# Kernel optimization log

Measured on AMD Instinct MI355X. Metric: run time of the kernel, lower is better.

The kernel has to match this reference:

```python
import jax, jax.numpy as jnp
import numpy as np

B, S, T, D = 4, 512, 512, 256


def setup_inputs() -> dict:
    key = jax.random.key(0)
    ks = jax.random.split(key, 10)
    scale = 1.0 / np.sqrt(D)
    return {
        "source": jax.random.normal(ks[0], (B, S, D), jnp.float32),
        "target": jax.random.normal(ks[1], (B, T, D), jnp.float32),
        "W_src": jax.random.uniform(ks[2], (D, D), jnp.float32, -scale, scale),
        "b_src": jax.random.uniform(ks[3], (D,), jnp.float32, -scale, scale),
        "W_tgt": jax.random.uniform(ks[4], (D, D), jnp.float32, -scale, scale),
        "b_tgt": jax.random.uniform(ks[5], (D,), jnp.float32, -scale, scale),
        "W_res": jax.random.uniform(ks[6], (D, 1), jnp.float32, -scale, scale),
        "b_res": jax.random.uniform(ks[7], (1,), jnp.float32, -scale, scale),
        "W_prob": jax.random.uniform(ks[8], (D, 2), jnp.float32, -scale, scale),
        "b_prob": jax.random.uniform(ks[9], (2,), jnp.float32, -scale, scale),
    }


def reference(source, target, W_src, b_src, W_tgt, b_tgt, W_res, b_res, W_prob, b_prob):
    # source: (B,S,D), target: (B,T,D)
    src_lin = jnp.einsum("bsd,de->bse", source, W_src) + b_src  # (B,S,D)
    tgt_lin = jnp.einsum("btd,de->bte", target, W_tgt) + b_tgt  # (B,T,D)
    # Bahdanau-style additive attention: (B,T,S,D) broadcast, tanh, D->1
    h = jnp.tanh(src_lin[:, None, :, :] + tgt_lin[:, :, None, :])  # (B,T,S,D)
    genP = jnp.einsum("btsd,d->bts", h, W_res[:, 0]) + b_res[0]     # (B,T,S)
    prob = jax.nn.softmax(jnp.einsum("btd,de->bte", target, W_prob) + b_prob, axis=-1)  # (B,T,2)
    return genP, prob
```

## Files before the change

kernel.cpp:

```cpp
#include <hip/hip_runtime.h>

#define B_ 4
#define S_ 512
#define T_ 512
#define D_ 256
#define NSRC (B_ * S_)
#define NROW 4096
#define K2F 2.8853900817779268f

typedef __attribute__((ext_vector_type(8))) short short8;
typedef __attribute__((ext_vector_type(4))) float f32x4;
typedef __attribute__((ext_vector_type(2))) float f32x2;

__device__ __forceinline__ unsigned short f2bf(float f) {
    union { float f; unsigned u; } v; v.f = f;
    unsigned r = v.u + 0x7FFF + ((v.u >> 16) & 1);
    return (unsigned short)(r >> 16);
}

__global__ __launch_bounds__(256) void prep_kernel(
    const float* __restrict__ tgt,
    const float* __restrict__ Wsrc, const float* __restrict__ Wtgt,
    const float* __restrict__ Wp, const float* __restrict__ bp,
    unsigned short* __restrict__ wtb, float* __restrict__ out)
{
    __shared__ float tl[64 * 65];
    const int blk = blockIdx.x, tid = threadIdx.x;

    if (blk < 32) {
        int wb = blk;
        int e = wb >> 4, ti = wb & 15, tr = ti >> 2, tc = ti & 3;
        int r0 = tr * 64, c0 = tc * 64;
        const float* W = e ? Wtgt : Wsrc;
        #pragma unroll
        for (int it = 0; it < 4; it++) {
            int rr = (tid >> 4) + it * 16;
            int cc = (tid & 15) * 4;
            float4 v = *(const float4*)&W[(r0 + rr) * D_ + c0 + cc];
            tl[(cc + 0) * 65 + rr] = v.x;
            tl[(cc + 1) * 65 + rr] = v.y;
            tl[(cc + 2) * 65 + rr] = v.z;
            tl[(cc + 3) * 65 + rr] = v.w;
        }
        __syncthreads();
        #pragma unroll
        for (int it = 0; it < 2; it++) {
            int jj = (tid >> 3) + it * 32;
            int kk = (tid & 7) * 8;
            ushort4 lo, hi;
            lo.x = f2bf(tl[jj * 65 + kk + 0]); lo.y = f2bf(tl[jj * 65 + kk + 1]);
            lo.z = f2bf(tl[jj * 65 + kk + 2]); lo.w = f2bf(tl[jj * 65 + kk + 3]);
            hi.x = f2bf(tl[jj * 65 + kk + 4]); hi.y = f2bf(tl[jj * 65 + kk + 5]);
            hi.z = f2bf(tl[jj * 65 + kk + 6]); hi.w = f2bf(tl[jj * 65 + kk + 7]);
            int idx = (e * 256 + c0 + jj) * D_ + r0 + kk;
            *(ushort4*)&wtb[idx] = lo;
            *(ushort4*)&wtb[idx + 4] = hi;
        }
    } else {
        int row  = (blk - 32) * 4 + (tid >> 6);
        int lane = tid & 63;
        float p0 = 0.f, p1 = 0.f;
        #pragma unroll
        for (int i = 0; i < 4; i++) {
            int d = lane + i * 64;
            float v = tgt[row * D_ + d];
            float2 w = *(const float2*)&Wp[d * 2];
            p0 = fmaf(v, w.x, p0);
            p1 = fmaf(v, w.y, p1);
        }
        #pragma unroll
        for (int off = 32; off > 0; off >>= 1) {
            p0 += __shfl_down(p0, off, 64);
            p1 += __shfl_down(p1, off, 64);
        }
        if (lane == 0) {
            const float L2E = 1.4426950408889634f;
            float l0 = p0 + bp[0], l1 = p1 + bp[1];
            float e10 = __builtin_amdgcn_exp2f((l1 - l0) * L2E);
            float e01 = __builtin_amdgcn_exp2f((l0 - l1) * L2E);
            out[B_ * T_ * S_ + row * 2 + 0] = __builtin_amdgcn_rcpf(1.f + e10);
            out[B_ * T_ * S_ + row * 2 + 1] = __builtin_amdgcn_rcpf(1.f + e01);
        }
    }
}

__global__ __launch_bounds__(256) void ysyt_kernel(
    const float* __restrict__ src, const float* __restrict__ tgt,
    const unsigned short* __restrict__ wtb,
    const float* __restrict__ bsrc, const float* __restrict__ btgt,
    float* __restrict__ yst)
{
    const int bx = blockIdx.x;
    const int rowblk = bx >> 2, colq = bx & 3;
    const int R0 = rowblk * 64;
    const int tid = threadIdx.x, lane = tid & 63, w = tid >> 6;
    const int n = lane & 15, quad = lane >> 4;
    const int mat = (R0 >= NSRC) ? 1 : 0;
    const float* bias = mat ? btgt : bsrc;
    const unsigned short* wtbase = wtb + mat * 256 * D_;
    const float* xb = mat ? &tgt[(R0 - NSRC) * D_] : &src[R0 * D_];

    short8 af[8];
    #pragma unroll
    for (int ks = 0; ks < 8; ks++) {
        const float* p = &xb[(w * 16 + n) * D_ + ks * 32 + quad * 8];
        float4 u0 = *(const float4*)p;
        float4 u1 = *(const float4*)(p + 4);
        short8 v;
        v[0] = (short)f2bf(u0.x); v[1] = (short)f2bf(u0.y);
        v[2] = (short)f2bf(u0.z); v[3] = (short)f2bf(u0.w);
        v[4] = (short)f2bf(u1.x); v[5] = (short)f2bf(u1.y);
        v[6] = (short)f2bf(u1.z); v[7] = (short)f2bf(u1.w);
        af[ks] = v;
    }

    #pragma unroll
    for (int gc = 0; gc < 4; gc++) {
        const int gcol = colq * 4 + gc;
        const unsigned short* bptr = &wtbase[(gcol * 16 + n) * D_ + quad * 8];
        short8 bf[8];
        #pragma unroll
        for (int ks = 0; ks < 8; ks++) bf[ks] = *(const short8*)&bptr[ks * 32];
        f32x4 a4 = {0.f, 0.f, 0.f, 0.f};
        #pragma unroll
        for (int ks = 0; ks < 8; ks++)
            a4 = __builtin_amdgcn_mfma_f32_16x16x32_bf16(af[ks], bf[ks], a4, 0, 0, 0);
        const float bv = bias[gcol * 16 + n];
        float4 o;
        o.x = __builtin_amdgcn_exp2f((a4[0] + bv) * K2F);
        o.y = __builtin_amdgcn_exp2f((a4[1] + bv) * K2F);
        o.z = __builtin_amdgcn_exp2f((a4[2] + bv) * K2F);
        o.w = __builtin_amdgcn_exp2f((a4[3] + bv) * K2F);
        *(float4*)&yst[(gcol * 16 + n) * NROW + R0 + w * 16 + quad * 4] = o;
    }
}

#define CLS 36
__global__ __launch_bounds__(256) void genp_kernel(
    const float* __restrict__ yst,
    const float* __restrict__ Wres, const float* __restrict__ bres,
    float* __restrict__ out)
{
    __shared__ float lys[2][64][CLS];
    __shared__ float lyt[2][64][CLS];
    __shared__ float c0s;

    const int tid = threadIdx.x;
    const int lane = tid & 63, w = tid >> 6;
    const int s0 = blockIdx.x * 32;
    const int t0 = blockIdx.y * 32;
    const int b  = blockIdx.z;
    const int m = tid & 15;
    const int g = tid >> 4;
    const int r = tid >> 3;
    const int q = tid & 7;

    if (w == 0) {
        float s = Wres[lane] + Wres[lane + 64] + Wres[lane + 128] + Wres[lane + 192];
        #pragma unroll
        for (int off = 32; off > 0; off >>= 1) s += __shfl_xor(s, off, 64);
        if (lane == 0) c0s = s + bres[0];
    }

    const int ysbase = b * S_ + s0;
    const int ytbase = NSRC + b * T_ + t0;

    {
        float4 a0 = *(const float4*)&yst[(r)      * NROW + ysbase + 4 * q];
        float4 a1 = *(const float4*)&yst[(r + 32) * NROW + ysbase + 4 * q];
        float4 b0 = *(const float4*)&yst[(r)      * NROW + ytbase + 4 * q];
        float4 b1 = *(const float4*)&yst[(r + 32) * NROW + ytbase + 4 * q];
        *(float4*)&lys[0][r][4 * q]      = a0;
        *(float4*)&lys[0][r + 32][4 * q] = a1;
        *(float4*)&lyt[0][r][4 * q]      = b0;
        *(float4*)&lyt[0][r + 32][4 * q] = b1;
    }
    __syncthreads();

    f32x2 acc[2];
    acc[0] = (f32x2){0.f, 0.f};
    acc[1] = (f32x2){0.f, 0.f};
    const f32x2 one2 = {1.f, 1.f};

    for (int c = 0; c < 4; c++) {
        const int bi = c & 1;
        float4 pa0, pa1, pb0, pb1;
        if (c < 3) {
            const int dn = (c + 1) * 64;
            pa0 = *(const float4*)&yst[(dn + r)      * NROW + ysbase + 4 * q];
            pa1 = *(const float4*)&yst[(dn + r + 32) * NROW + ysbase + 4 * q];
            pb0 = *(const float4*)&yst[(dn + r)      * NROW + ytbase + 4 * q];
            pb1 = *(const float4*)&yst[(dn + r + 32) * NROW + ytbase + 4 * q];
        }

        const float* wp = &Wres[c * 64];
        #pragma unroll 2
        for (int kq = 0; kq < 8; kq++) {
            const int d0 = 8 * kq;
            f32x2 ap[8];
            float2 ct[8];
            f32x2 wv[8];
            #pragma unroll
            for (int k = 0; k < 8; k++) {
                float2 a2 = *(const float2*)&lys[bi][d0 + k][2 * m];
                ct[k] = *(const float2*)&lyt[bi][d0 + k][2 * g];
                ap[k] = (f32x2){a2.x, a2.y};
                const float wk = wp[d0 + k];
                wv[k] = (f32x2){wk, wk};
            }
            #pragma unroll
            for (int i = 0; i < 2; i++) {
                const float c0 = i ? ct[0].y : ct[0].x;
                f32x2 dd[8];
                #pragma unroll
                for (int k = 0; k < 8; k++) {
                    const float cv = i ? ct[k].y : ct[k].x;
                    const f32x2 cs = {cv, cv};
                    dd[k] = ap[k] * cs + one2;
                }
                f32x2 p01 = dd[0] * dd[1];
                f32x2 p23 = dd[2] * dd[3];
                f32x2 p45 = dd[4] * dd[5];
                f32x2 p67 = dd[6] * dd[7];
                f32x2 q03 = p01 * p23;
                f32x2 q47 = p45 * p67;
                f32x2 den = q03 * q47;
                f32x2 u01 = dd[1] * wv[0]; u01 = dd[0] * wv[1] + u01;
                f32x2 u23 = dd[3] * wv[2]; u23 = dd[2] * wv[3] + u23;
                f32x2 u45 = dd[5] * wv[4]; u45 = dd[4] * wv[5] + u45;
                f32x2 u67 = dd[7] * wv[6]; u67 = dd[6] * wv[7] + u67;
                f32x2 n03 = u01 * p23; n03 = u23 * p01 + n03;
                f32x2 n47 = u45 * p67; n47 = u67 * p45 + n47;
                f32x2 num = n03 * q47; num = n47 * q03 + num;
                f32x2 rr;
                rr.x = __builtin_amdgcn_rcpf(den.x);
                rr.y = __builtin_amdgcn_rcpf(den.y);
                acc[i] = num * rr + acc[i];
                (void)c0;
            }
        }

        if (c < 3) {
            *(float4*)&lys[bi ^ 1][r][4 * q]      = pa0;
            *(float4*)&lys[bi ^ 1][r + 32][4 * q] = pa1;
            *(float4*)&lyt[bi ^ 1][r][4 * q]      = pb0;
            *(float4*)&lyt[bi ^ 1][r + 32][4 * q] = pb1;
        }
        __syncthreads();
    }

    const float C0 = c0s;
    #pragma unroll
    for (int i = 0; i < 2; i++) {
        float2 o;
        o.x = C0 - 2.f * acc[i].x;
        o.y = C0 - 2.f * acc[i].y;
        *(float2*)&out[(b * T_ + t0 + 2 * g + i) * S_ + s0 + 2 * m] = o;
    }
}

extern "C" void kernel_launch(void* const* d_in, const int* in_sizes, int n_in,
                              void* d_out, int out_size, void* d_ws, size_t ws_size,
                              hipStream_t stream) {
    const float* source = (const float*)d_in[0];
    const float* target = (const float*)d_in[1];
    const float* W_src  = (const float*)d_in[2];
    const float* b_src  = (const float*)d_in[3];
    const float* W_tgt  = (const float*)d_in[4];
    const float* b_tgt  = (const float*)d_in[5];
    const float* W_res  = (const float*)d_in[6];
    const float* b_res  = (const float*)d_in[7];
    const float* W_prob = (const float*)d_in[8];
    const float* b_prob = (const float*)d_in[9];
    float* out = (float*)d_out;

    unsigned short* wtb = (unsigned short*)d_ws;
    float* yst = (float*)((char*)d_ws + 256 * 1024);

    prep_kernel<<<544, 256, 0, stream>>>(target, W_src, W_tgt,
                                         W_prob, b_prob, wtb, out);
    ysyt_kernel<<<256, 256, 0, stream>>>(source, target, wtb,
                                         b_src, b_tgt, yst);
    genp_kernel<<<dim3(16, 16, 4), 256, 0, stream>>>(yst, W_res, b_res, out);
}
```

Measured before the change: 107.1 us.

## Store target projections row-major and read them as wave-uniform scalars in genp

The ysyt kernel now writes the target projection transposed through shared memory into a row-major buffer, so each wave in genp can load its four target rows with uniform (scalar) float4 loads instead of staging them in LDS. The genp tile changes from 32x32 to 128 source by 16 target positions: each lane handles two source columns and each wave four target rows. This removes the LDS traffic and bank pressure from the target operand and halves the number of LDS arrays. In exchange there are more global loads from the target buffer inside the inner loop and a larger LDS footprint per block.

```diff
diff --git a/kernel.cpp b/kernel.cpp
--- a/kernel.cpp
+++ b/kernel.cpp
@@ -5,7 +5,6 @@
 #define T_ 512
 #define D_ 256
 #define NSRC (B_ * S_)
-#define NROW 4096
 #define K2F 2.8853900817779268f
 
 typedef __attribute__((ext_vector_type(8))) short short8;
@@ -88,8 +87,9 @@
     const float* __restrict__ src, const float* __restrict__ tgt,
     const unsigned short* __restrict__ wtb,
     const float* __restrict__ bsrc, const float* __restrict__ btgt,
-    float* __restrict__ yst)
+    float* __restrict__ yst, float* __restrict__ ytp)
 {
+    __shared__ float lt[64][68];
     const int bx = blockIdx.x;
     const int rowblk = bx >> 2, colq = bx & 3;
     const int R0 = rowblk * 64;
@@ -131,29 +131,43 @@
         o.y = __builtin_amdgcn_exp2f((a4[1] + bv) * K2F);
         o.z = __builtin_amdgcn_exp2f((a4[2] + bv) * K2F);
         o.w = __builtin_amdgcn_exp2f((a4[3] + bv) * K2F);
-        *(float4*)&yst[(gcol * 16 + n) * NROW + R0 + w * 16 + quad * 4] = o;
-    }
-}
-
-#define CLS 36
+        if (mat == 0) {
+            *(float4*)&yst[(gcol * 16 + n) * NSRC + R0 + w * 16 + quad * 4] = o;
+        } else {
+            const int rl = w * 16 + quad * 4;
+            const int dl = gc * 16 + n;
+            lt[rl + 0][dl] = o.x;
+            lt[rl + 1][dl] = o.y;
+            lt[rl + 2][dl] = o.z;
+            lt[rl + 3][dl] = o.w;
+        }
+    }
+    if (mat == 1) {
+        __syncthreads();
+        const int row = tid >> 2, seg = tid & 3;
+        const int tg = R0 - NSRC + row;
+        #pragma unroll
+        for (int i = 0; i < 4; i++) {
+            *(float4*)&ytp[tg * D_ + colq * 64 + seg * 16 + 4 * i] =
+                *(const float4*)&lt[row][seg * 16 + 4 * i];
+        }
+    }
+}
+
 __global__ __launch_bounds__(256) void genp_kernel(
     const float* __restrict__ yst,
+    const float* __restrict__ ytp,
     const float* __restrict__ Wres, const float* __restrict__ bres,
     float* __restrict__ out)
 {
-    __shared__ float lys[2][64][CLS];
-    __shared__ float lyt[2][64][CLS];
+    __shared__ float lys[2][64][128];
     __shared__ float c0s;
 
     const int tid = threadIdx.x;
     const int lane = tid & 63, w = tid >> 6;
-    const int s0 = blockIdx.x * 32;
-    const int t0 = blockIdx.y * 32;
+    const int s0 = blockIdx.x * 128;
+    const int t0 = blockIdx.y * 16;
     const int b  = blockIdx.z;
-    const int m = tid & 15;
-    const int g = tid >> 4;
-    const int r = tid >> 3;
-    const int q = tid & 7;
 
     if (w == 0) {
         float s = Wres[lane] + Wres[lane + 64] + Wres[lane + 128] + Wres[lane + 192];
@@ -162,60 +176,66 @@
         if (lane == 0) c0s = s + bres[0];
     }
 
-    const int ysbase = b * S_ + s0;
-    const int ytbase = NSRC + b * T_ + t0;
+    const int wu = __builtin_amdgcn_readfirstlane(w);
+    const float* ytb0 = ytp + (b * 512 + t0 + wu * 4) * D_;
+    const int cbase = b * 512 + s0;
+
+    const int sfi = tid * 8;
+    const int srow = sfi >> 5;
+    const int scol = (sfi & 31) * 4;
 
     {
-        float4 a0 = *(const float4*)&yst[(r)      * NROW + ysbase + 4 * q];
-        float4 a1 = *(const float4*)&yst[(r + 32) * NROW + ysbase + 4 * q];
-        float4 b0 = *(const float4*)&yst[(r)      * NROW + ytbase + 4 * q];
-        float4 b1 = *(const float4*)&yst[(r + 32) * NROW + ytbase + 4 * q];
-        *(float4*)&lys[0][r][4 * q]      = a0;
-        *(float4*)&lys[0][r + 32][4 * q] = a1;
-        *(float4*)&lyt[0][r][4 * q]      = b0;
-        *(float4*)&lyt[0][r + 32][4 * q] = b1;
+        #pragma unroll
+        for (int j = 0; j < 8; j++) {
+            const int fr = srow + ((scol + 4 * j) >> 7);
+            const int fc = (scol + 4 * j) & 127;
+            *(float4*)&lys[0][fr][fc] = *(const float4*)&yst[fr * NSRC + cbase + fc];
+        }
     }
     __syncthreads();
 
-    f32x2 acc[2];
-    acc[0] = (f32x2){0.f, 0.f};
-    acc[1] = (f32x2){0.f, 0.f};
+    f32x2 acc[4];
+    #pragma unroll
+    for (int i = 0; i < 4; i++) acc[i] = (f32x2){0.f, 0.f};
     const f32x2 one2 = {1.f, 1.f};
 
     for (int c = 0; c < 4; c++) {
         const int bi = c & 1;
-        float4 pa0, pa1, pb0, pb1;
+        float4 pf[8];
         if (c < 3) {
-            const int dn = (c + 1) * 64;
-            pa0 = *(const float4*)&yst[(dn + r)      * NROW + ysbase + 4 * q];
-            pa1 = *(const float4*)&yst[(dn + r + 32) * NROW + ysbase + 4 * q];
-            pb0 = *(const float4*)&yst[(dn + r)      * NROW + ytbase + 4 * q];
-            pb1 = *(const float4*)&yst[(dn + r + 32) * NROW + ytbase + 4 * q];
+            #pragma unroll
+            for (int j = 0; j < 8; j++) {
+                const int fr = srow + ((scol + 4 * j) >> 7);
+                const int fc = (scol + 4 * j) & 127;
+                pf[j] = *(const float4*)&yst[((c + 1) * 64 + fr) * NSRC + cbase + fc];
+            }
         }
 
         const float* wp = &Wres[c * 64];
+        const float* ytb = ytb0 + c * 64;
         #pragma unroll 2
         for (int kq = 0; kq < 8; kq++) {
             const int d0 = 8 * kq;
             f32x2 ap[8];
-            float2 ct[8];
             f32x2 wv[8];
             #pragma unroll
             for (int k = 0; k < 8; k++) {
-                float2 a2 = *(const float2*)&lys[bi][d0 + k][2 * m];
-                ct[k] = *(const float2*)&lyt[bi][d0 + k][2 * g];
+                float2 a2 = *(const float2*)&lys[bi][d0 + k][2 * lane];
                 ap[k] = (f32x2){a2.x, a2.y};
                 const float wk = wp[d0 + k];
                 wv[k] = (f32x2){wk, wk};
             }
             #pragma unroll
-            for (int i = 0; i < 2; i++) {
-                const float c0 = i ? ct[0].y : ct[0].x;
+            for (int tt = 0; tt < 4; tt++) {
+                const float* tp = ytb + tt * D_ + d0;
+                float4 c0v = *(const float4*)&tp[0];
+                float4 c1v = *(const float4*)&tp[4];
+                const float ctv[8] = {c0v.x, c0v.y, c0v.z, c0v.w,
+                                      c1v.x, c1v.y, c1v.z, c1v.w};
                 f32x2 dd[8];
                 #pragma unroll
                 for (int k = 0; k < 8; k++) {
-                    const float cv = i ? ct[k].y : ct[k].x;
-                    const f32x2 cs = {cv, cv};
+                    const f32x2 cs = {ctv[k], ctv[k]};
                     dd[k] = ap[k] * cs + one2;
                 }
                 f32x2 p01 = dd[0] * dd[1];
@@ -235,27 +255,28 @@
                 f32x2 rr;
                 rr.x = __builtin_amdgcn_rcpf(den.x);
                 rr.y = __builtin_amdgcn_rcpf(den.y);
-                acc[i] = num * rr + acc[i];
-                (void)c0;
+                acc[tt] = num * rr + acc[tt];
             }
         }
 
         if (c < 3) {
-            *(float4*)&lys[bi ^ 1][r][4 * q]      = pa0;
-            *(float4*)&lys[bi ^ 1][r + 32][4 * q] = pa1;
-            *(float4*)&lyt[bi ^ 1][r][4 * q]      = pb0;
-            *(float4*)&lyt[bi ^ 1][r + 32][4 * q] = pb1;
+            #pragma unroll
+            for (int j = 0; j < 8; j++) {
+                const int fr = srow + ((scol + 4 * j) >> 7);
+                const int fc = (scol + 4 * j) & 127;
+                *(float4*)&lys[bi ^ 1][fr][fc] = pf[j];
+            }
         }
         __syncthreads();
     }
 
     const float C0 = c0s;
     #pragma unroll
-    for (int i = 0; i < 2; i++) {
+    for (int tt = 0; tt < 4; tt++) {
         float2 o;
-        o.x = C0 - 2.f * acc[i].x;
-        o.y = C0 - 2.f * acc[i].y;
-        *(float2*)&out[(b * T_ + t0 + 2 * g + i) * S_ + s0 + 2 * m] = o;
+        o.x = C0 - 2.f * acc[tt].x;
+        o.y = C0 - 2.f * acc[tt].y;
+        *(float2*)&out[(b * T_ + t0 + wu * 4 + tt) * S_ + s0 + 2 * lane] = o;
     }
 }
 
@@ -276,10 +297,11 @@
 
     unsigned short* wtb = (unsigned short*)d_ws;
     float* yst = (float*)((char*)d_ws + 256 * 1024);
+    float* ytp = yst + 256 * NSRC;
 
     prep_kernel<<<544, 256, 0, stream>>>(target, W_src, W_tgt,
                                          W_prob, b_prob, wtb, out);
     ysyt_kernel<<<256, 256, 0, stream>>>(source, target, wtb,
-                                         b_src, b_tgt, yst);
-    genp_kernel<<<dim3(16, 16, 4), 256, 0, stream>>>(yst, W_res, b_res, out);
-}
+                                         b_src, b_tgt, yst, ytp);
+    genp_kernel<<<dim3(4, 32, 4), 256, 0, stream>>>(yst, ytp, W_res, b_res, out);
+}
```

After: 121.1 us. +13.0%, slower.

## Fuse weight transpose/bf16 conversion into projection kernel via shared memory

Applied to the files above, without the earlier changes.

Removes the separate prep kernel that transposed and converted W_src/W_tgt to bf16 in global workspace. Each projection block now loads its own 64-column slice of the fp32 weight, converts it to bf16 and stores it transposed in LDS, then feeds MFMA from LDS. The prob softmax rows run as extra blocks in the same launch. This drops one kernel launch and a global round trip, but each block now redoes the weight conversion (64 redundant reads of each weight slice) and uses 32KB of LDS per block.

```diff
diff --git a/kernel.cpp b/kernel.cpp
--- a/kernel.cpp
+++ b/kernel.cpp
@@ -18,55 +18,85 @@
     return (unsigned short)(r >> 16);
 }
 
-__global__ __launch_bounds__(256) void prep_kernel(
-    const float* __restrict__ tgt,
+__global__ __launch_bounds__(256) void ysyt_kernel(
+    const float* __restrict__ src, const float* __restrict__ tgt,
     const float* __restrict__ Wsrc, const float* __restrict__ Wtgt,
-    const float* __restrict__ Wp, const float* __restrict__ bp,
-    unsigned short* __restrict__ wtb, float* __restrict__ out)
+    const float* __restrict__ Wp,  const float* __restrict__ bp,
+    const float* __restrict__ bsrc, const float* __restrict__ btgt,
+    float* __restrict__ yst, float* __restrict__ out)
 {
-    __shared__ float tl[64 * 65];
-    const int blk = blockIdx.x, tid = threadIdx.x;
-
-    if (blk < 32) {
-        int wb = blk;
-        int e = wb >> 4, ti = wb & 15, tr = ti >> 2, tc = ti & 3;
-        int r0 = tr * 64, c0 = tc * 64;
-        const float* W = e ? Wtgt : Wsrc;
-        #pragma unroll
-        for (int it = 0; it < 4; it++) {
-            int rr = (tid >> 4) + it * 16;
-            int cc = (tid & 15) * 4;
-            float4 v = *(const float4*)&W[(r0 + rr) * D_ + c0 + cc];
-            tl[(cc + 0) * 65 + rr] = v.x;
-            tl[(cc + 1) * 65 + rr] = v.y;
-            tl[(cc + 2) * 65 + rr] = v.z;
-            tl[(cc + 3) * 65 + rr] = v.w;
+    __shared__ unsigned short lwt[16384];
+    const int bid = blockIdx.x, tid = threadIdx.x;
+    const int lane = tid & 63, w = tid >> 6;
+
+    if (bid < 256) {
+        const int rowblk = bid >> 2, colq = bid & 3;
+        const int R0 = rowblk * 64;
+        const int n = lane & 15, quad = lane >> 4;
+        const int mat = (R0 >= NSRC) ? 1 : 0;
+        const float* bias = mat ? btgt : bsrc;
+        const float* Wm = mat ? Wtgt : Wsrc;
+        const float* xb = mat ? &tgt[(R0 - NSRC) * D_] : &src[R0 * D_];
+
+        {
+            const int r = tid;
+            const int ksr = r >> 5, qr = (r >> 3) & 3, jr = r & 7;
+            const int wbase = ksr * 512 + qr * 8 + jr;
+            #pragma unroll 4
+            for (int i = 0; i < 16; i++) {
+                float4 v = *(const float4*)&Wm[r * D_ + colq * 64 + 4 * i];
+                const int cc = 4 * i;
+                lwt[((cc + 0) >> 4) * 4096 + ((cc + 0) & 15) * 32 + wbase] = f2bf(v.x);
+                lwt[((cc + 1) >> 4) * 4096 + ((cc + 1) & 15) * 32 + wbase] = f2bf(v.y);
+                lwt[((cc + 2) >> 4) * 4096 + ((cc + 2) & 15) * 32 + wbase] = f2bf(v.z);
+                lwt[((cc + 3) >> 4) * 4096 + ((cc + 3) & 15) * 32 + wbase] = f2bf(v.w);
+            }
+        }
+
+        short8 af[8];
+        #pragma unroll
+        for (int ks = 0; ks < 8; ks++) {
+            const float* p = &xb[(w * 16 + n) * D_ + ks * 32 + quad * 8];
+            float4 u0 = *(const float4*)p;
+            float4 u1 = *(const float4*)(p + 4);
+            short8 v;
+            v[0] = (short)f2bf(u0.x); v[1] = (short)f2bf(u0.y);
+            v[2] = (short)f2bf(u0.z); v[3] = (short)f2bf(u0.w);
+            v[4] = (short)f2bf(u1.x); v[5] = (short)f2bf(u1.y);
+            v[6] = (short)f2bf(u1.z); v[7] = (short)f2bf(u1.w);
+            af[ks] = v;
         }
         __syncthreads();
-        #pragma unroll
-        for (int it = 0; it < 2; it++) {
-            int jj = (tid >> 3) + it * 32;
-            int kk = (tid & 7) * 8;
-            ushort4 lo, hi;
-            lo.x = f2bf(tl[jj * 65 + kk + 0]); lo.y = f2bf(tl[jj * 65 + kk + 1]);
-            lo.z = f2bf(tl[jj * 65 + kk + 2]); lo.w = f2bf(tl[jj * 65 + kk + 3]);
-            hi.x = f2bf(tl[jj * 65 + kk + 4]); hi.y = f2bf(tl[jj * 65 + kk + 5]);
-            hi.z = f2bf(tl[jj * 65 + kk + 6]); hi.w = f2bf(tl[jj * 65 + kk + 7]);
-            int idx = (e * 256 + c0 + jj) * D_ + r0 + kk;
-            *(ushort4*)&wtb[idx] = lo;
-            *(ushort4*)&wtb[idx + 4] = hi;
+
+        #pragma unroll
+        for (int gc = 0; gc < 4; gc++) {
+            const int gcol = colq * 4 + gc;
+            const unsigned short* bp2 = &lwt[gc * 4096 + n * 32 + quad * 8];
+            short8 bf[8];
+            #pragma unroll
+            for (int ks = 0; ks < 8; ks++) bf[ks] = *(const short8*)&bp2[ks * 512];
+            f32x4 a4 = {0.f, 0.f, 0.f, 0.f};
+            #pragma unroll
+            for (int ks = 0; ks < 8; ks++)
+                a4 = __builtin_amdgcn_mfma_f32_16x16x32_bf16(af[ks], bf[ks], a4, 0, 0, 0);
+            const float bv = bias[gcol * 16 + n];
+            float4 o;
+            o.x = __builtin_amdgcn_exp2f((a4[0] + bv) * K2F);
+            o.y = __builtin_amdgcn_exp2f((a4[1] + bv) * K2F);
+            o.z = __builtin_amdgcn_exp2f((a4[2] + bv) * K2F);
+            o.w = __builtin_amdgcn_exp2f((a4[3] + bv) * K2F);
+            *(float4*)&yst[(gcol * 16 + n) * NROW + R0 + w * 16 + quad * 4] = o;
         }
     } else {
-        int row  = (blk - 32) * 4 + (tid >> 6);
-        int lane = tid & 63;
+        int row  = (bid - 256) * 4 + w;
         float p0 = 0.f, p1 = 0.f;
         #pragma unroll
         for (int i = 0; i < 4; i++) {
             int d = lane + i * 64;
             float v = tgt[row * D_ + d];
-            float2 w = *(const float2*)&Wp[d * 2];
-            p0 = fmaf(v, w.x, p0);
-            p1 = fmaf(v, w.y, p1);
+            float2 wv = *(const float2*)&Wp[d * 2];
+            p0 = fmaf(v, wv.x, p0);
+            p1 = fmaf(v, wv.y, p1);
         }
         #pragma unroll
         for (int off = 32; off > 0; off >>= 1) {
@@ -81,57 +111,6 @@
             out[B_ * T_ * S_ + row * 2 + 0] = __builtin_amdgcn_rcpf(1.f + e10);
             out[B_ * T_ * S_ + row * 2 + 1] = __builtin_amdgcn_rcpf(1.f + e01);
         }
-    }
-}
-
-__global__ __launch_bounds__(256) void ysyt_kernel(
-    const float* __restrict__ src, const float* __restrict__ tgt,
-    const unsigned short* __restrict__ wtb,
-    const float* __restrict__ bsrc, const float* __restrict__ btgt,
-    float* __restrict__ yst)
-{
-    const int bx = blockIdx.x;
-    const int rowblk = bx >> 2, colq = bx & 3;
-    const int R0 = rowblk * 64;
-    const int tid = threadIdx.x, lane = tid & 63, w = tid >> 6;
-    const int n = lane & 15, quad = lane >> 4;
-    const int mat = (R0 >= NSRC) ? 1 : 0;
-    const float* bias = mat ? btgt : bsrc;
-    const unsigned short* wtbase = wtb + mat * 256 * D_;
-    const float* xb = mat ? &tgt[(R0 - NSRC) * D_] : &src[R0 * D_];
-
-    short8 af[8];
-    #pragma unroll
-    for (int ks = 0; ks < 8; ks++) {
-        const float* p = &xb[(w * 16 + n) * D_ + ks * 32 + quad * 8];
-        float4 u0 = *(const float4*)p;
-        float4 u1 = *(const float4*)(p + 4);
-        short8 v;
-        v[0] = (short)f2bf(u0.x); v[1] = (short)f2bf(u0.y);
-        v[2] = (short)f2bf(u0.z); v[3] = (short)f2bf(u0.w);
-        v[4] = (short)f2bf(u1.x); v[5] = (short)f2bf(u1.y);
-        v[6] = (short)f2bf(u1.z); v[7] = (short)f2bf(u1.w);
-        af[ks] = v;
-    }
-
-    #pragma unroll
-    for (int gc = 0; gc < 4; gc++) {
-        const int gcol = colq * 4 + gc;
-        const unsigned short* bptr = &wtbase[(gcol * 16 + n) * D_ + quad * 8];
-        short8 bf[8];
-        #pragma unroll
-        for (int ks = 0; ks < 8; ks++) bf[ks] = *(const short8*)&bptr[ks * 32];
-        f32x4 a4 = {0.f, 0.f, 0.f, 0.f};
-        #pragma unroll
-        for (int ks = 0; ks < 8; ks++)
-            a4 = __builtin_amdgcn_mfma_f32_16x16x32_bf16(af[ks], bf[ks], a4, 0, 0, 0);
-        const float bv = bias[gcol * 16 + n];
-        float4 o;
-        o.x = __builtin_amdgcn_exp2f((a4[0] + bv) * K2F);
-        o.y = __builtin_amdgcn_exp2f((a4[1] + bv) * K2F);
-        o.z = __builtin_amdgcn_exp2f((a4[2] + bv) * K2F);
-        o.w = __builtin_amdgcn_exp2f((a4[3] + bv) * K2F);
-        *(float4*)&yst[(gcol * 16 + n) * NROW + R0 + w * 16 + quad * 4] = o;
     }
 }
 
@@ -274,12 +253,10 @@
     const float* b_prob = (const float*)d_in[9];
     float* out = (float*)d_out;
 
-    unsigned short* wtb = (unsigned short*)d_ws;
-    float* yst = (float*)((char*)d_ws + 256 * 1024);
-
-    prep_kernel<<<544, 256, 0, stream>>>(target, W_src, W_tgt,
-                                         W_prob, b_prob, wtb, out);
-    ysyt_kernel<<<256, 256, 0, stream>>>(source, target, wtb,
-                                         b_src, b_tgt, yst);
+    float* yst = (float*)d_ws;
+
+    ysyt_kernel<<<768, 256, 0, stream>>>(source, target, W_src, W_tgt,
+                                         W_prob, b_prob, b_src, b_tgt,
+                                         yst, out);
     genp_kernel<<<dim3(16, 16, 4), 256, 0, stream>>>(yst, W_res, b_res, out);
 }
```

After: 105.5 us (median of 2 runs). Within noise of the previous version (-1.5%).
